# Performance work log

Measured on AMD Instinct MI355X. Metric: run time of the kernel, lower is better.

## Reference

```python
import jax, jax.numpy as jnp
import numpy as np

# constants from VMD_block.__init__ (K=4, alpha=2000, tau=0, DC=0, init=1, tol=5e-5, max_N=5)
K = 4
ALPHA = 2000.0
TAU = 0.0
TOL = 5e-05
MAX_N = 5


def _mvmd(f):
    """Multivariate VMD (Rehman & Aftab 2019) on f: (C, T) real signals.
    Returns modes u: (K, C, T). Shared center frequencies omega across channels."""
    C, T = f.shape
    half = T // 2
    T2 = 2 * T
    # mirror extension to length 2T
    fM = jnp.concatenate([f[:, :half][:, ::-1], f, f[:, half:][:, ::-1]], axis=1)
    freqs = (jnp.arange(1, T2 + 1, dtype=f.dtype) / T2) - 0.5 - (1.0 / T2)  # (T2,)
    f_hat = jnp.fft.fftshift(jnp.fft.fft(fM, axis=1), axes=1).astype(jnp.complex64)
    h2 = T2 // 2
    f_hat_plus = f_hat.at[:, :h2].set(0.0)  # keep analytic (positive-freq) part
    fpos = freqs[h2:]

    omega0 = (0.5 / K) * jnp.arange(K, dtype=f.dtype)  # init == 1, DC == 0
    u0 = jnp.zeros((K, C, T2), dtype=jnp.complex64)
    lam0 = jnp.zeros((C, T2), dtype=jnp.complex64)

    def cond(st):
        _, _, _, n, uDiff = st
        return jnp.logical_and(uDiff > TOL, n < MAX_N)

    def body(st):
        u, omega, lam, n, _ = st
        u_prev = u
        sum_all = jnp.sum(u, axis=0)  # (C, T2)
        for k in range(K):  # Gauss-Seidel mode updates; K is small & static
            sum_uk = sum_all - u[k]
            denom = 1.0 + ALPHA * (freqs - omega[k]) ** 2  # (T2,)
            u_k = (f_hat_plus - sum_uk - lam / 2.0) / denom
            sum_all = sum_uk + u_k
            u = u.at[k].set(u_k)
            power = jnp.abs(u_k[:, h2:]) ** 2  # (C, T2/2) positive freqs
            omega = omega.at[k].set(jnp.sum(fpos * power) / jnp.sum(power))
        lam = lam + TAU * (sum_all - f_hat_plus)  # tau == 0 -> dual ascent is a no-op
        d = u - u_prev
        uDiff = jnp.abs(jnp.sum(d * jnp.conj(d)) / T2) + jnp.finfo(jnp.float32).eps
        return u, omega, lam, n + 1, uDiff.astype(jnp.float32)

    st0 = (u0, omega0, lam0, jnp.int32(0), jnp.float32(TOL + 1.0))
    u, omega, lam, n, uDiff = jax.lax.while_loop(cond, body, st0)

    # rebuild full spectrum via Hermitian symmetry, back to time domain
    u_hat = jnp.zeros((K, C, T2), dtype=jnp.complex64)
    u_hat = u_hat.at[:, :, h2:].set(u[:, :, h2:])
    u_hat = u_hat.at[:, :, 1:h2 + 1].set(jnp.conj(u[:, :, h2:])[:, :, ::-1])
    u_hat = u_hat.at[:, :, 0].set(jnp.conj(u_hat[:, :, -1]))
    ut = jnp.real(jnp.fft.ifft(jnp.fft.ifftshift(u_hat, axes=-1), axis=-1))
    return ut[:, :, T2 // 4: 3 * T2 // 4]  # crop mirror padding -> (K, C, T)


def setup_inputs() -> dict:
    key = jax.random.key(0)
    x = jax.random.normal(key, (8, 2048, 64), dtype=jnp.float32)  # (B, T, C)
    return {"x": x}


def reference(x):
    B, T, C = x.shape
    xr = jnp.transpose(x, (0, 2, 1)).reshape(B * C, T)  # (B*C, T)
    u = _mvmd(xr)  # (K, B*C, T)
    x_l = jnp.transpose(u[0].reshape(B, C, T), (0, 2, 1))  # lowest-freq mode -> (B, T, C)
    x_h = x - x_l
    return (x_h, x_l)
```

## Files before the change

kernel.cpp:

```cpp
#include <hip/hip_runtime.h>
#include <math.h>

#define NBLK 512
#define EPS32 1.1920928955078125e-07

__device__ __forceinline__ double ld_acc(const double* p){
  return __hip_atomic_load(p, __ATOMIC_RELAXED, __HIP_MEMORY_SCOPE_AGENT);
}
__device__ __forceinline__ unsigned ld_u32(const unsigned* p){
  return __hip_atomic_load(p, __ATOMIC_RELAXED, __HIP_MEMORY_SCOPE_AGENT);
}
__device__ __forceinline__ void st_u32(unsigned* p, unsigned v){
  __hip_atomic_store(p, v, __ATOMIC_RELAXED, __HIP_MEMORY_SCOPE_AGENT);
}

__device__ void tree_sync_omega(unsigned* leaf, unsigned* root, unsigned* rec,
                                const double* slot, float* somf, int gid){
  unsigned old = __hip_atomic_fetch_add(leaf + (size_t)gid * 32, 1u,
                                        __ATOMIC_RELAXED, __HIP_MEMORY_SCOPE_AGENT);
  if (old == 63u){
    unsigned oldr = __hip_atomic_fetch_add(root, 1u,
                                           __ATOMIC_RELAXED, __HIP_MEMORY_SCOPE_AGENT);
    if (oldr == 7u){
      double uD = ld_acc(slot + 8);
      float o0 = (float)(ld_acc(slot + 0) / ld_acc(slot + 4));
      float o1 = (float)(ld_acc(slot + 1) / ld_acc(slot + 5));
      float o2 = (float)(ld_acc(slot + 2) / ld_acc(slot + 6));
      float o3 = (float)(ld_acc(slot + 3) / ld_acc(slot + 7));
      unsigned fl = (uD * (1.0 / 4096.0) + EPS32 > 5e-5) ? 3u : 1u;
      st_u32(rec + 1, __float_as_uint(o0));
      st_u32(rec + 2, __float_as_uint(o1));
      st_u32(rec + 3, __float_as_uint(o2));
      st_u32(rec + 4, __float_as_uint(o3));
      __hip_atomic_store(rec, fl, __ATOMIC_RELEASE, __HIP_MEMORY_SCOPE_AGENT);
    }
  }
  unsigned f, spins = 0;
  while (((f = ld_u32(rec)) & 1u) == 0u){
    if (++spins > (1u << 22)) break;
    __builtin_amdgcn_s_sleep(2);
  }
  somf[7] = (f & 2u) ? 1.f : 0.f;
  somf[0] = __uint_as_float(ld_u32(rec + 1));
  somf[1] = __uint_as_float(ld_u32(rec + 2));
  somf[2] = __uint_as_float(ld_u32(rec + 3));
  somf[3] = __uint_as_float(ld_u32(rec + 4));
}

#define R4REG(A, B, C, D, W1, W2, W3, SGN, Y0, Y1, Y2, Y3) {    \
  float w1y_ = (SGN)*W1.y, w2y_ = (SGN)*W2.y, w3y_ = (SGN)*W3.y;\
  float t0x = A.x + C.x, t0y = A.y + C.y;                       \
  float t1x = A.x - C.x, t1y = A.y - C.y;                       \
  float t2x = B.x + D.x, t2y = B.y + D.y;                       \
  float t3x = (SGN) * (B.y - D.y), t3y = -(SGN) * (B.x - D.x);  \
  Y0 = make_float2(t0x + t2x, t0y + t2y);                       \
  float y1x = t1x + t3x, y1y = t1y + t3y;                       \
  float y2x = t0x - t2x, y2y = t0y - t2y;                       \
  float y3x = t1x - t3x, y3y = t1y - t3y;                       \
  Y1 = make_float2(y1x*W1.x - y1y*w1y_, y1x*w1y_ + y1y*W1.x);   \
  Y2 = make_float2(y2x*W2.x - y2y*w2y_, y2x*w2y_ + y2y*W2.x);   \
  Y3 = make_float2(y3x*W3.x - y3y*w3y_, y3x*w3y_ + y3y*W3.x); }

__device__ __forceinline__ void r4s(float2* src, float2* dst,
                                    const float2* twl, float sgn, int cnt){
  const int tid = threadIdx.x;
  #pragma unroll 1
  for (int t = 0; t < cnt; ++t){
    const int L = 4 << (2 * t);
    const int Lm = L - 1;
    int q  = tid & Lm;
    int tb = tid - q;
    float2 a = src[tid];
    float2 b = src[tid + 256];
    float2 c = src[tid + 512];
    float2 d = src[tid + 768];
    float2 w1 = twl[tb];
    float2 w2 = twl[2 * tb];
    float2 w3 = twl[3 * tb];
    float2 y0, y1, y2, y3;
    R4REG(a, b, c, d, w1, w2, w3, sgn, y0, y1, y2, y3)
    int ob = q + (tb << 2);
    dst[ob]         = y0;
    dst[ob + L]     = y1;
    dst[ob + 2 * L] = y2;
    dst[ob + 3 * L] = y3;
    __syncthreads();
    float2* tt = src; src = dst; dst = tt;
  }
}

__device__ __forceinline__ float wredf(float v){
  #pragma unroll
  for (int off = 32; off; off >>= 1) v += __shfl_down(v, off);
  return v;
}

__device__ __forceinline__ void red9(float a0, float a1, float a2, float a3,
                                     float a4, float a5, float a6, float a7,
                                     float a8, float* redf, double* accs){
  const int tid = threadIdx.x, wave = tid >> 6, lane = tid & 63;
  float r;
  r = wredf(a0); if (lane == 0) redf[ 0 + wave] = r;
  r = wredf(a1); if (lane == 0) redf[ 4 + wave] = r;
  r = wredf(a2); if (lane == 0) redf[ 8 + wave] = r;
  r = wredf(a3); if (lane == 0) redf[12 + wave] = r;
  r = wredf(a4); if (lane == 0) redf[16 + wave] = r;
  r = wredf(a5); if (lane == 0) redf[20 + wave] = r;
  r = wredf(a6); if (lane == 0) redf[24 + wave] = r;
  r = wredf(a7); if (lane == 0) redf[28 + wave] = r;
  r = wredf(a8); if (lane == 0) redf[32 + wave] = r;
  __syncthreads();
  if (tid < 9){
    double s = (double)redf[tid*4+0] + (double)redf[tid*4+1]
             + (double)redf[tid*4+2] + (double)redf[tid*4+3];
    atomicAdd(&accs[tid], s);
  }
}

#define MODE_R(RC, OMC, AFP, AP) {                             \
  float o_ = s - (RC);                                         \
  float d_ = fj - (OMC);                                       \
  float rd_ = __builtin_amdgcn_rcpf(fmaf(2000.0f*d_, d_, 1.0f));\
  float n_ = (RR - o_) * rd_;                                  \
  float pw_ = n_ * n_;                                         \
  AFP += fj * pw_;  AP += pw_;                                 \
  float dd_ = n_ - (RC);  aD += dd_ * dd_;                     \
  (RC) = n_;  s = o_ + n_; }

#define RBIN(RHO, RRv, FJ) {                                   \
  float RR = RRv;  float fj = FJ;                              \
  float s = RHO.x + RHO.y + RHO.z + RHO.w;                     \
  MODE_R(RHO.x, om.x, aFP0, aP0)                               \
  MODE_R(RHO.y, om.y, aFP1, aP1)                               \
  MODE_R(RHO.z, om.z, aFP2, aP2)                               \
  MODE_R(RHO.w, om.w, aFP3, aP3) }

#define IT1R(RHO, RRv, FJ) { RHO = make_float4(0.f,0.f,0.f,0.f); RBIN(RHO, RRv, FJ) }

#define FOR8R(M) M(r0,R0,fj0) M(r1,R1,fj1) M(r2,R2,fj2) M(r3,R3,fj3) \
                 M(r4,R4,fj4) M(r5,R5,fj5) M(r6,R6,fj6) M(r7,R7,fj7)

#define C5(RHO, RRv, FJ, CV) {                                 \
  if (act){                                                    \
    float o_ = RHO.y + RHO.z + RHO.w;                          \
    float d_ = FJ - om0;                                       \
    float rd_ = __builtin_amdgcn_rcpf(fmaf(2000.0f*d_, d_, 1.0f));\
    CV = (RRv - o_) * rd_;                                     \
  } else CV = RHO.x; }

__global__ void __attribute__((amdgpu_flat_work_group_size(256, 256),
                               amdgpu_waves_per_eu(2, 2)))
k_main(const float* __restrict__ x, unsigned* __restrict__ leaf,
       unsigned* __restrict__ root, unsigned* __restrict__ rec,
       double* __restrict__ accs, float* __restrict__ xh, float* __restrict__ xl){
  __shared__ float2 twl[768];
  __shared__ float2 bufA[1024];
  __shared__ float2 bufB[1024];
  __shared__ float redf[36];
  __shared__ float somf[8];
  __shared__ float2 vNy;
  __shared__ float sKs;
  const int tid = threadIdx.x;
  const int b = blockIdx.x & 7, ch = blockIdx.x >> 3;
  const int gid = blockIdx.x & 7;
  const float* xc = x + (size_t)b * 2048 * 64 + ch;

  #pragma unroll
  for (int i = 0; i < 3; ++i){
    int p = tid + (i << 8);
    float rev = (float)p * (-1.0f / 1024.0f);
    twl[p] = make_float2(__builtin_amdgcn_cosf(rev), __builtin_amdgcn_sinf(rev));
  }

  float2 za = make_float2(xc[(size_t)(4*tid       ) * 64], xc[(size_t)(4*tid + 2   ) * 64]);
  float2 zb = make_float2(xc[(size_t)(4*tid + 1024) * 64], xc[(size_t)(4*tid + 1026) * 64]);
  float2 zc = make_float2(xc[(size_t)(2047 - 4*tid) * 64], xc[(size_t)(2045 - 4*tid) * 64]);
  float2 zd = make_float2(xc[(size_t)(1023 - 4*tid) * 64], xc[(size_t)(1021 - 4*tid) * 64]);
  __syncthreads();

  {
    float2 w1 = twl[tid], w2 = twl[2*tid], w3 = twl[3*tid];
    float2 y0, y1, y2, y3;
    R4REG(za, zb, zc, zd, w1, w2, w3, 1.0f, y0, y1, y2, y3)
    float4* d4 = reinterpret_cast<float4*>(bufA + 4 * tid);
    d4[0] = make_float4(y0.x, y0.y, y1.x, y1.y);
    d4[1] = make_float4(y2.x, y2.y, y3.x, y3.y);
  }
  __syncthreads();
  r4s(bufA, bufB, twl, 1.0f, 4);

  float R0,R1,R2,R3,R4,R5,R6,R7, fj0,fj1,fj2,fj3,fj4,fj5,fj6,fj7;
  #define UNPK(C, RA, RB, FA, FB) {                            \
    int k = tid + ((C) << 8);                                  \
    float2 Zk = bufA[k];                                       \
    float2 Zm = bufA[(1024 - k) & 1023];                       \
    float px = 0.5f*(Zk.x + Zm.x), py = 0.5f*(Zk.y - Zm.y);    \
    float qx = 0.5f*(Zk.x - Zm.x), qy = 0.5f*(Zk.y + Zm.y);    \
    float rw = (float)k * (-1.0f / 2048.0f);                   \
    float Wx = __builtin_amdgcn_cosf(rw), Wy = __builtin_amdgcn_sinf(rw); \
    float Vx = px + Wx*qy + Wy*qx;                             \
    float Vy = py - Wx*qx + Wy*qy;                             \
    float re = (float)k * (-1.0f / 8192.0f);                   \
    float Ex = __builtin_amdgcn_cosf(re), Ey = __builtin_amdgcn_sinf(re); \
    RA = 2.0f * (Ex*Vx - Ey*Vy);                               \
    RB = -2.0f * (Ex*Vy + Ey*Vx);                              \
    FA = (float)k * (1.0f/4096.0f);                            \
    FB = (float)(2048 - k) * (1.0f/4096.0f); }
  UNPK(0, R0, R1, fj0, fj1)
  UNPK(1, R2, R3, fj2, fj3)
  UNPK(2, R4, R5, fj4, fj5)
  UNPK(3, R6, R7, fj6, fj7)
  if (tid == 0){
    float2 Z0 = bufA[0];
    R1 = 1.41421356237f * (Z0.x - Z0.y);
    fj1 = 0.25f;
  }

  float4 r0, r1, r2, r3, r4, r5, r6, r7;
  float4 om = make_float4(0.0f, 0.125f, 0.25f, 0.375f);

  {
    float aFP0=0,aFP1=0,aFP2=0,aFP3=0,aP0=0,aP1=0,aP2=0,aP3=0,aD=0;
    FOR8R(IT1R)
    red9(aFP0,aFP1,aFP2,aFP3,aP0,aP1,aP2,aP3,aD, redf, accs);
  }

  bool active = true;
  #pragma unroll 1
  for (int it = 0; it < 3; ++it){
    __syncthreads();
    if (tid == 0)
      tree_sync_omega(leaf + it * 256, root + it * 32, rec + it * 32,
                      accs + it * 16, somf, gid);
    __syncthreads();
    if (active){
      if (somf[7] != 0.0f){
        om.x = somf[0]; om.y = somf[1]; om.z = somf[2]; om.w = somf[3];
      } else active = false;
    }
    if (active){
      float aFP0=0,aFP1=0,aFP2=0,aFP3=0,aP0=0,aP1=0,aP2=0,aP3=0,aD=0;
      FOR8R(RBIN)
      red9(aFP0,aFP1,aFP2,aFP3,aP0,aP1,aP2,aP3,aD, redf, accs + (it + 1) * 16);
    }
  }
  __syncthreads();
  if (tid == 0)
    tree_sync_omega(leaf + 3 * 256, root + 3 * 32, rec + 3 * 32,
                    accs + 3 * 16, somf, gid);
  __syncthreads();

  {
    bool act = active && (somf[7] != 0.0f);
    float om0 = somf[0];
    float c0, c1, c2, c3, c4, c5, c6, c7;
    C5(r0, R0, fj0, c0)  C5(r1, R1, fj1, c1)
    C5(r2, R2, fj2, c2)  C5(r3, R3, fj3, c3)
    C5(r4, R4, fj4, c4)  C5(r5, R5, fj5, c5)
    C5(r6, R6, fj6, c6)  C5(r7, R7, fj7, c7)
    if (tid == 1) sKs = c1;
    if (tid == 0) vNy = make_float2(1.41421356237f * c1, 0.0f);
    #define VPW(C, CA, CB) {                                   \
      int k = tid + ((C) << 8);                                \
      float rg = (float)k * (1.0f / 8192.0f);                  \
      float Gx = __builtin_amdgcn_cosf(rg), Gy = __builtin_amdgcn_sinf(rg); \
      bufA[k] = make_float2(Gx*(CA) + Gy*(CB), Gy*(CA) - Gx*(CB)); }
    VPW(0, c0, c1)  VPW(1, c2, c3)  VPW(2, c4, c5)  VPW(3, c6, c7)
    if (tid == 0) bufA[0] = make_float2(c0, 0.0f);
  }
  __syncthreads();
  float2 p0, p1, p2, p3;
  #define ZB(C, ZV) {                                          \
    int q = tid + ((C) << 8);                                  \
    float2 Vq = bufA[q];                                       \
    float2 Vm = (q == 0) ? vNy : bufA[1024 - q];               \
    Vm.y = -Vm.y;                                              \
    float Ex_ = Vq.x + Vm.x, Ey_ = Vq.y + Vm.y;                \
    float Dx = Vq.x - Vm.x,  Dy = Vq.y - Vm.y;                 \
    float rw = (float)q * (1.0f / 2048.0f);                    \
    float Wx = __builtin_amdgcn_cosf(rw), Wy = __builtin_amdgcn_sinf(rw); \
    float Ox = Dx*Wx - Dy*Wy;                                  \
    float Oy = Dx*Wy + Dy*Wx;                                  \
    ZV = make_float2(Ex_ - Oy, Ey_ + Ox); }
  ZB(0, p0)  ZB(1, p1)  ZB(2, p2)  ZB(3, p3)
  {
    float2 w1 = twl[tid], w2 = twl[2*tid], w3 = twl[3*tid];
    float2 y0, y1, y2, y3;
    R4REG(p0, p1, p2, p3, w1, w2, w3, -1.0f, y0, y1, y2, y3)
    float4* d4 = reinterpret_cast<float4*>(bufB + 4 * tid);
    d4[0] = make_float4(y0.x, y0.y, y1.x, y1.y);
    d4[1] = make_float4(y2.x, y2.y, y3.x, y3.y);
  }
  __syncthreads();
  r4s(bufB, bufA, twl, -1.0f, 3);

  {
    float2 a = bufA[tid], bb = bufA[tid + 256];
    float2 c = bufA[tid + 512], d = bufA[tid + 768];
    float t0x = a.x + c.x, t0y = a.y + c.y;
    float t1x = a.x - c.x, t1y = a.y - c.y;
    float t2x = bb.x + d.x, t2y = bb.y + d.y;
    float t3x = -(bb.y - d.y), t3y = (bb.x - d.x);
    float2 y0 = make_float2(t0x + t2x, t0y + t2y);
    float2 y1 = make_float2(t1x + t3x, t1y + t3y);
    float2 y2 = make_float2(t0x - t2x, t0y - t2y);
    float2 y3 = make_float2(t1x - t3x, t1y - t3y);
    const float sc = 1.0f / 4096.0f;
    float kc = sKs * (0.99999970586f * sc);
    #define OUT2(YV, T0, T1, KS, ZS) {                         \
      size_t oa = ((size_t)(b * 2048 + (T0))) * 64 + ch;       \
      size_t ob = ((size_t)(b * 2048 + (T1))) * 64 + ch;       \
      float l0 = YV.x * sc KS kc;                              \
      float l1 = YV.y * sc KS kc;                              \
      xl[oa] = l0;  xh[oa] = ZS.x - l0;                        \
      xl[ob] = l1;  xh[ob] = ZS.y - l1; }
    OUT2(y0, 4*tid,        4*tid + 2,    -, za)
    OUT2(y1, 4*tid + 1024, 4*tid + 1026, -, zb)
    OUT2(y2, 2047 - 4*tid, 2045 - 4*tid, +, zc)
    OUT2(y3, 1023 - 4*tid, 1021 - 4*tid, +, zd)
  }
}

extern "C" void kernel_launch(void* const* d_in, const int* in_sizes, int n_in,
                              void* d_out, int out_size, void* d_ws, size_t ws_size,
                              hipStream_t stream){
  const float* x = (const float*)d_in[0];
  float* out_xh = (float*)d_out;
  float* out_xl = out_xh + (size_t)8 * 2048 * 64;

  char* ws = (char*)d_ws;
  unsigned* leaf = (unsigned*)ws;
  unsigned* root = (unsigned*)(ws + 4096);
  unsigned* rec  = (unsigned*)(ws + 4608);
  double*   accs = (double*)  (ws + 5120);

  hipMemsetAsync(ws, 0, 5632, stream);
  k_main<<<NBLK, 256, 0, stream>>>(x, leaf, root, rec, accs, out_xh, out_xl);
}
```

Before: 118.7 us.

## Use three-level grid barrier with sharded accumulators and replicated release flags

Replaces the two-level cross-block barrier with a three-level tree: leaf counters of 8 blocks, mid counters, and a root. The 9 reduction accumulators are split into 8 slots that the mid-level winners fold into a root accumulator. The omega result and flag are written to 8 replicated records so pollers spread across cache lines, and the sleep interval is shortened. This targets atomic contention on hot addresses during the grid-wide sync, at the cost of more atomics and a larger workspace memset. The last radix-4 FFT stage is also kept in registers and feeds the unpack directly, which saves one shared-memory round trip.

```diff
diff --git a/kernel.cpp b/kernel.cpp
--- a/kernel.cpp
+++ b/kernel.cpp
@@ -14,37 +14,58 @@
   __hip_atomic_store(p, v, __ATOMIC_RELAXED, __HIP_MEMORY_SCOPE_AGENT);
 }
 
-__device__ void tree_sync_omega(unsigned* leaf, unsigned* root, unsigned* rec,
-                                const double* slot, float* somf, int gid){
-  unsigned old = __hip_atomic_fetch_add(leaf + (size_t)gid * 32, 1u,
-                                        __ATOMIC_RELAXED, __HIP_MEMORY_SCOPE_AGENT);
-  if (old == 63u){
-    unsigned oldr = __hip_atomic_fetch_add(root, 1u,
-                                           __ATOMIC_RELAXED, __HIP_MEMORY_SCOPE_AGENT);
-    if (oldr == 7u){
-      double uD = ld_acc(slot + 8);
-      float o0 = (float)(ld_acc(slot + 0) / ld_acc(slot + 4));
-      float o1 = (float)(ld_acc(slot + 1) / ld_acc(slot + 5));
-      float o2 = (float)(ld_acc(slot + 2) / ld_acc(slot + 6));
-      float o3 = (float)(ld_acc(slot + 3) / ld_acc(slot + 7));
-      unsigned fl = (uD * (1.0 / 4096.0) + EPS32 > 5e-5) ? 3u : 1u;
-      st_u32(rec + 1, __float_as_uint(o0));
-      st_u32(rec + 2, __float_as_uint(o1));
-      st_u32(rec + 3, __float_as_uint(o2));
-      st_u32(rec + 4, __float_as_uint(o3));
-      __hip_atomic_store(rec, fl, __ATOMIC_RELEASE, __HIP_MEMORY_SCOPE_AGENT);
+__device__ void tree_sync_omega(unsigned* leafL, unsigned* midL, unsigned* rootL,
+                                unsigned* recL, const double* accsG,
+                                double* racc, float* somf, int l6, int g3){
+  unsigned o = __hip_atomic_fetch_add(leafL + (size_t)l6 * 32, 1u,
+                                      __ATOMIC_RELAXED, __HIP_MEMORY_SCOPE_AGENT);
+  if (o == 7u){
+    int m = l6 & 7;
+    unsigned om_ = __hip_atomic_fetch_add(midL + (size_t)m * 32, 1u,
+                                          __ATOMIC_RELAXED, __HIP_MEMORY_SCOPE_AGENT);
+    if (om_ == 7u){
+      const double* ag = accsG + (size_t)m * 16;
+      double v0 = ld_acc(ag+0), v1 = ld_acc(ag+1), v2 = ld_acc(ag+2);
+      double v3 = ld_acc(ag+3), v4 = ld_acc(ag+4), v5 = ld_acc(ag+5);
+      double v6 = ld_acc(ag+6), v7 = ld_acc(ag+7), v8 = ld_acc(ag+8);
+      atomicAdd(racc+0, v0); atomicAdd(racc+1, v1); atomicAdd(racc+2, v2);
+      atomicAdd(racc+3, v3); atomicAdd(racc+4, v4); atomicAdd(racc+5, v5);
+      atomicAdd(racc+6, v6); atomicAdd(racc+7, v7); atomicAdd(racc+8, v8);
+      unsigned orr = __hip_atomic_fetch_add(rootL, 1u,
+                                            __ATOMIC_ACQ_REL, __HIP_MEMORY_SCOPE_AGENT);
+      if (orr == 7u){
+        double uD = ld_acc(racc + 8);
+        float o0 = (float)(ld_acc(racc+0) / ld_acc(racc+4));
+        float o1 = (float)(ld_acc(racc+1) / ld_acc(racc+5));
+        float o2 = (float)(ld_acc(racc+2) / ld_acc(racc+6));
+        float o3 = (float)(ld_acc(racc+3) / ld_acc(racc+7));
+        unsigned fl = (uD * (1.0 / 4096.0) + EPS32 > 5e-5) ? 3u : 1u;
+        #pragma unroll
+        for (int r = 0; r < 8; ++r){
+          unsigned* rl = recL + (size_t)r * 32;
+          st_u32(rl + 1, __float_as_uint(o0));
+          st_u32(rl + 2, __float_as_uint(o1));
+          st_u32(rl + 3, __float_as_uint(o2));
+          st_u32(rl + 4, __float_as_uint(o3));
+        }
+        #pragma unroll
+        for (int r = 0; r < 8; ++r)
+          __hip_atomic_store(recL + (size_t)r * 32, fl,
+                             __ATOMIC_RELEASE, __HIP_MEMORY_SCOPE_AGENT);
+      }
     }
   }
+  unsigned* myrec = recL + (size_t)g3 * 32;
   unsigned f, spins = 0;
-  while (((f = ld_u32(rec)) & 1u) == 0u){
+  while (((f = ld_u32(myrec)) & 1u) == 0u){
     if (++spins > (1u << 22)) break;
-    __builtin_amdgcn_s_sleep(2);
+    __builtin_amdgcn_s_sleep(1);
   }
   somf[7] = (f & 2u) ? 1.f : 0.f;
-  somf[0] = __uint_as_float(ld_u32(rec + 1));
-  somf[1] = __uint_as_float(ld_u32(rec + 2));
-  somf[2] = __uint_as_float(ld_u32(rec + 3));
-  somf[3] = __uint_as_float(ld_u32(rec + 4));
+  somf[0] = __uint_as_float(ld_u32(myrec + 1));
+  somf[1] = __uint_as_float(ld_u32(myrec + 2));
+  somf[2] = __uint_as_float(ld_u32(myrec + 3));
+  somf[3] = __uint_as_float(ld_u32(myrec + 4));
 }
 
 #define R4REG(A, B, C, D, W1, W2, W3, SGN, Y0, Y1, Y2, Y3) {    \
@@ -97,7 +118,7 @@
 
 __device__ __forceinline__ void red9(float a0, float a1, float a2, float a3,
                                      float a4, float a5, float a6, float a7,
-                                     float a8, float* redf, double* accs){
+                                     float a8, float* redf, double* accsG){
   const int tid = threadIdx.x, wave = tid >> 6, lane = tid & 63;
   float r;
   r = wredf(a0); if (lane == 0) redf[ 0 + wave] = r;
@@ -113,7 +134,7 @@
   if (tid < 9){
     double s = (double)redf[tid*4+0] + (double)redf[tid*4+1]
              + (double)redf[tid*4+2] + (double)redf[tid*4+3];
-    atomicAdd(&accs[tid], s);
+    atomicAdd(&accsG[tid], s);
   }
 }
 
@@ -151,7 +172,8 @@
 __global__ void __attribute__((amdgpu_flat_work_group_size(256, 256),
                                amdgpu_waves_per_eu(2, 2)))
 k_main(const float* __restrict__ x, unsigned* __restrict__ leaf,
-       unsigned* __restrict__ root, unsigned* __restrict__ rec,
+       unsigned* __restrict__ mid, unsigned* __restrict__ root,
+       unsigned* __restrict__ rec, double* __restrict__ racc,
        double* __restrict__ accs, float* __restrict__ xh, float* __restrict__ xl){
   __shared__ float2 twl[768];
   __shared__ float2 bufA[1024];
@@ -162,7 +184,7 @@
   __shared__ float sKs;
   const int tid = threadIdx.x;
   const int b = blockIdx.x & 7, ch = blockIdx.x >> 3;
-  const int gid = blockIdx.x & 7;
+  const int l6 = blockIdx.x & 63, g3 = blockIdx.x & 7;
   const float* xc = x + (size_t)b * 2048 * 64 + ch;
 
   #pragma unroll
@@ -187,12 +209,28 @@
     d4[1] = make_float4(y2.x, y2.y, y3.x, y3.y);
   }
   __syncthreads();
-  r4s(bufA, bufB, twl, 1.0f, 4);
+  r4s(bufA, bufB, twl, 1.0f, 3);
+  float2 Zs0, Zs1, Zs2, Zs3;
+  {
+    float2 a = bufB[tid], b2 = bufB[tid + 256];
+    float2 c2 = bufB[tid + 512], d2 = bufB[tid + 768];
+    float t0x = a.x + c2.x, t0y = a.y + c2.y;
+    float t1x = a.x - c2.x, t1y = a.y - c2.y;
+    float t2x = b2.x + d2.x, t2y = b2.y + d2.y;
+    float t3x = (b2.y - d2.y), t3y = -(b2.x - d2.x);
+    Zs0 = make_float2(t0x + t2x, t0y + t2y);
+    Zs1 = make_float2(t1x + t3x, t1y + t3y);
+    Zs2 = make_float2(t0x - t2x, t0y - t2y);
+    Zs3 = make_float2(t1x - t3x, t1y - t3y);
+    bufA[tid]       = Zs0;  bufA[tid + 256] = Zs1;
+    bufA[tid + 512] = Zs2;  bufA[tid + 768] = Zs3;
+  }
+  __syncthreads();
 
   float R0,R1,R2,R3,R4,R5,R6,R7, fj0,fj1,fj2,fj3,fj4,fj5,fj6,fj7;
-  #define UNPK(C, RA, RB, FA, FB) {                            \
+  #define UNPK(C, ZS, RA, RB, FA, FB) {                        \
     int k = tid + ((C) << 8);                                  \
-    float2 Zk = bufA[k];                                       \
+    float2 Zk = ZS;                                            \
     float2 Zm = bufA[(1024 - k) & 1023];                       \
     float px = 0.5f*(Zk.x + Zm.x), py = 0.5f*(Zk.y - Zm.y);    \
     float qx = 0.5f*(Zk.x - Zm.x), qy = 0.5f*(Zk.y + Zm.y);    \
@@ -206,13 +244,12 @@
     RB = -2.0f * (Ex*Vy + Ey*Vx);                              \
     FA = (float)k * (1.0f/4096.0f);                            \
     FB = (float)(2048 - k) * (1.0f/4096.0f); }
-  UNPK(0, R0, R1, fj0, fj1)
-  UNPK(1, R2, R3, fj2, fj3)
-  UNPK(2, R4, R5, fj4, fj5)
-  UNPK(3, R6, R7, fj6, fj7)
+  UNPK(0, Zs0, R0, R1, fj0, fj1)
+  UNPK(1, Zs1, R2, R3, fj2, fj3)
+  UNPK(2, Zs2, R4, R5, fj4, fj5)
+  UNPK(3, Zs3, R6, R7, fj6, fj7)
   if (tid == 0){
-    float2 Z0 = bufA[0];
-    R1 = 1.41421356237f * (Z0.x - Z0.y);
+    R1 = 1.41421356237f * (Zs0.x - Zs0.y);
     fj1 = 0.25f;
   }
 
@@ -222,7 +259,7 @@
   {
     float aFP0=0,aFP1=0,aFP2=0,aFP3=0,aP0=0,aP1=0,aP2=0,aP3=0,aD=0;
     FOR8R(IT1R)
-    red9(aFP0,aFP1,aFP2,aFP3,aP0,aP1,aP2,aP3,aD, redf, accs);
+    red9(aFP0,aFP1,aFP2,aFP3,aP0,aP1,aP2,aP3,aD, redf, accs + (size_t)g3*16);
   }
 
   bool active = true;
@@ -230,8 +267,10 @@
   for (int it = 0; it < 3; ++it){
     __syncthreads();
     if (tid == 0)
-      tree_sync_omega(leaf + it * 256, root + it * 32, rec + it * 32,
-                      accs + it * 16, somf, gid);
+      tree_sync_omega(leaf + (size_t)it*64*32, mid + (size_t)it*8*32,
+                      root + (size_t)it*32, rec + (size_t)it*8*32,
+                      accs + (size_t)it*128, racc + (size_t)it*16,
+                      somf, l6, g3);
     __syncthreads();
     if (active){
       if (somf[7] != 0.0f){
@@ -241,13 +280,16 @@
     if (active){
       float aFP0=0,aFP1=0,aFP2=0,aFP3=0,aP0=0,aP1=0,aP2=0,aP3=0,aD=0;
       FOR8R(RBIN)
-      red9(aFP0,aFP1,aFP2,aFP3,aP0,aP1,aP2,aP3,aD, redf, accs + (it + 1) * 16);
+      red9(aFP0,aFP1,aFP2,aFP3,aP0,aP1,aP2,aP3,aD, redf,
+           accs + (size_t)(it + 1)*128 + (size_t)g3*16);
     }
   }
   __syncthreads();
   if (tid == 0)
-    tree_sync_omega(leaf + 3 * 256, root + 3 * 32, rec + 3 * 32,
-                    accs + 3 * 16, somf, gid);
+    tree_sync_omega(leaf + (size_t)3*64*32, mid + (size_t)3*8*32,
+                    root + (size_t)3*32, rec + (size_t)3*8*32,
+                    accs + (size_t)3*128, racc + (size_t)3*16,
+                    somf, l6, g3);
   __syncthreads();
 
   {
@@ -330,10 +372,13 @@
 
   char* ws = (char*)d_ws;
   unsigned* leaf = (unsigned*)ws;
-  unsigned* root = (unsigned*)(ws + 4096);
-  unsigned* rec  = (unsigned*)(ws + 4608);
-  double*   accs = (double*)  (ws + 5120);
-
-  hipMemsetAsync(ws, 0, 5632, stream);
-  k_main<<<NBLK, 256, 0, stream>>>(x, leaf, root, rec, accs, out_xh, out_xl);
-}
+  unsigned* mid  = (unsigned*)(ws + 32768);
+  unsigned* root = (unsigned*)(ws + 36864);
+  double*   racc = (double*)  (ws + 37376);
+  unsigned* rec  = (unsigned*)(ws + 37888);
+  double*   accs = (double*)  (ws + 41984);
+
+  hipMemsetAsync(ws, 0, 46080, stream);
+  k_main<<<NBLK, 256, 0, stream>>>(x, leaf, mid, root, rec, racc, accs,
+                                   out_xh, out_xl);
+}
```

Measured after the change: 112.3 us, median of 2. -5.4%, faster.
